# Kernel tuning notes

Hardware: AMD Instinct MI355X
Metric: run time of the kernel (lower is better)

## Reference

```python
import jax, jax.numpy as jnp
import numpy as np

J, F_ = 17, 32  # joints x per-joint features; C = J*F_ = 544
H = 8           # num_heads
EPS = 1e-5


def _layernorm(x, g, b):
    mu = jnp.mean(x, axis=-1, keepdims=True)
    var = jnp.mean((x - mu) ** 2, axis=-1, keepdims=True)
    return (x - mu) * jax.lax.rsqrt(var + EPS) * g + b


def setup_inputs() -> dict:
    key = jax.random.key(0)
    ks = jax.random.split(key, 8)
    B, N, C = 8, 1024, J * F_
    x = jax.random.normal(ks[0], (B, N, C), dtype=jnp.float32)
    s = 1.0 / np.sqrt(C)
    return {
        "x": x,
        "norm_g": jnp.ones((F_,), jnp.float32),
        "norm_b": jnp.zeros((F_,), jnp.float32),
        "ap_w": jax.random.normal(ks[1], (1, F_), jnp.float32) / np.sqrt(F_),
        "ap_b": jnp.zeros((1,), jnp.float32),
        "norm2_g": jnp.ones((C,), jnp.float32),
        "norm2_b": jnp.zeros((C,), jnp.float32),
        "qkv_w": jax.random.normal(ks[2], (3 * C, C), jnp.float32) * s,
        "proj_w": jax.random.normal(ks[3], (C, C), jnp.float32) * s,
        "proj_b": jnp.zeros((C,), jnp.float32),
        "scaling_factor": jnp.array([2.0], jnp.float32),
    }


def reference(x, norm_g, norm_b, ap_w, ap_b, norm2_g, norm2_b, qkv_w, proj_w, proj_b, scaling_factor):
    B, N, C = x.shape
    hd = C // H
    # --- attention pooling over joints ---
    xr = x.reshape(B, N, J, F_)
    xr = _layernorm(xr, norm_g, norm_b)                      # [B,N,17,32]
    scores = jnp.einsum('bnjf,of->bnjo', xr, ap_w)[..., 0] + ap_b[0]  # [B,N,17]
    # nn.Softmax(dim=1): softmax over sequence axis N (faithful to source)
    w = jax.nn.softmax(scores, axis=1)
    xp = (xr * w[..., None]).reshape(B, N, C)
    xp = _layernorm(xp, norm2_g, norm2_b)
    # --- position-scaled self-attention ---
    positions = jnp.linspace(0.0, 1.0, N, dtype=jnp.float32)  # [N]
    pos_scale = jnp.exp(-scaling_factor[0] * (positions - 0.5) ** 2)  # per-key scale
    qkv = (xp @ qkv_w.T).reshape(B, N, 3, H, hd)
    q = qkv[:, :, 0].transpose(0, 2, 1, 3)  # [B,H,N,hd]
    k = qkv[:, :, 1].transpose(0, 2, 1, 3)
    v = qkv[:, :, 2].transpose(0, 2, 1, 3)
    scale = hd ** -0.5
    attn = jnp.einsum('bhqd,bhkd->bhqk', q, k) * (scale * pos_scale[None, None, None, :])
    attn = jax.nn.softmax(attn, axis=-1)
    out = jnp.einsum('bhqk,bhkd->bhqd', attn, v)
    out = out.transpose(0, 2, 1, 3).reshape(B, N, C)
    return out @ proj_w.T + proj_b
```

## Files before the change

### kernel.cpp

```cpp
#include <hip/hip_runtime.h>
#include <hip/hip_bf16.h>

#define BB 8
#define NN 1024
#define CC 544
#define JJ 17
#define FF 32
#define HH 8
#define HD 68
#define BN 8192
#define KD 544
#define NCQ 1632
#define NCQP 1664
#define NCPP 640
#define NKB 9
#define BHSZ 73728
#define AQR 64

using f32x4  = __attribute__((ext_vector_type(4))) float;
using bf16x8 = __attribute__((ext_vector_type(8))) short;

__device__ __forceinline__ void gld_lds16(const void* g, void* l) {
  __builtin_amdgcn_global_load_lds(
      (const __attribute__((address_space(1))) void*)g,
      (__attribute__((address_space(3))) void*)l, 16, 0, 0);
}

__device__ __forceinline__ float bf16bits2f(short bits) {
  return __uint_as_float(((unsigned)(unsigned short)bits) << 16);
}

__global__ __launch_bounds__(256) void wconv_ln1(const float* __restrict__ x,
                                                 const float* __restrict__ g,
                                                 const float* __restrict__ bta,
                                                 const float* __restrict__ apw,
                                                 const float* __restrict__ apb,
                                                 __hip_bfloat16* __restrict__ xr,
                                                 float* __restrict__ scores,
                                                 const float* __restrict__ qkv_w,
                                                 const float* __restrict__ proj_w,
                                                 __hip_bfloat16* __restrict__ qw,
                                                 __hip_bfloat16* __restrict__ pw) {
  int bid = blockIdx.x, t = threadIdx.x;
  if (bid < BN / 4) {
    int wv = t >> 6, lane = t & 63;
    int bn = bid * 4 + wv;
    int f = lane & 31, half = lane >> 5;
    const float* row = x + (size_t)bn * CC;
    float gg = g[f], bb = bta[f], aw = apw[f], ab = apb[0];
    for (int it = 0; it < 9; ++it) {
      int j = it * 2 + half;
      bool act = (j < JJ);
      float v = act ? row[j * FF + f] : 0.f;
      float s = v;
      for (int m = 16; m >= 1; m >>= 1) s += __shfl_xor(s, m);
      float mu = s * (1.f / 32.f);
      float dv = v - mu;
      float s2 = dv * dv;
      for (int m = 16; m >= 1; m >>= 1) s2 += __shfl_xor(s2, m);
      float xn = dv * rsqrtf(s2 * (1.f / 32.f) + 1e-5f) * gg + bb;
      float sc = xn * aw;
      for (int m = 16; m >= 1; m >>= 1) sc += __shfl_xor(sc, m);
      if (act) {
        xr[(size_t)bn * CC + j * FF + f] = __float2bfloat16(xn);
        if (f == 0) scores[bn * JJ + j] = sc + ab;
      }
    }
  } else {
    int wb = bid - BN / 4;
    bool isq = wb < NCQP;
    int r = isq ? wb : wb - NCQP;
    const float* src = isq ? qkv_w : proj_w;
    __hip_bfloat16* dst = isq ? qw : pw;
    int nrows = isq ? NCQ : CC;
    if (t < KD / 4) {
      int c = t * 4;
      float4 v;
      if (r < nrows) v = *(const float4*)(src + (size_t)r * KD + c);
      else           v = float4{0.f, 0.f, 0.f, 0.f};
      __hip_bfloat16 o[4] = {__float2bfloat16(v.x), __float2bfloat16(v.y),
                             __float2bfloat16(v.z), __float2bfloat16(v.w)};
      *(unsigned long long*)(dst + (size_t)r * KD + c) = *(unsigned long long*)o;
    }
  }
}

__global__ __launch_bounds__(256) void softmax_red(const float* __restrict__ scores,
                                                   float2* __restrict__ tab) {
  int bj = blockIdx.x;
  int b = bj / JJ, j = bj - b * JJ;
  const float* s = scores + (size_t)b * NN * JJ + j;
  int t = threadIdx.x;
  float v[4];
  float mx = -1e30f;
#pragma unroll
  for (int i = 0; i < 4; ++i) { v[i] = s[(t + 256 * i) * JJ]; mx = fmaxf(mx, v[i]); }
#pragma unroll
  for (int m = 32; m >= 1; m >>= 1) mx = fmaxf(mx, __shfl_xor(mx, m));
  __shared__ float red[4];
  if ((t & 63) == 0) red[t >> 6] = mx;
  __syncthreads();
  mx = fmaxf(fmaxf(red[0], red[1]), fmaxf(red[2], red[3]));
  float sum = 0.f;
#pragma unroll
  for (int i = 0; i < 4; ++i) sum += __expf(v[i] - mx);
#pragma unroll
  for (int m = 32; m >= 1; m >>= 1) sum += __shfl_xor(sum, m);
  __shared__ float red2[4];
  if ((t & 63) == 0) red2[t >> 6] = sum;
  __syncthreads();
  if (t == 0) {
    sum = red2[0] + red2[1] + red2[2] + red2[3];
    tab[bj] = make_float2(mx, 1.f / sum);
  }
}

__global__ __launch_bounds__(256) void ln2_xp(const __hip_bfloat16* __restrict__ xr,
                                              const float* __restrict__ scores,
                                              const float2* __restrict__ tab,
                                              const float* __restrict__ g2,
                                              const float* __restrict__ b2,
                                              __hip_bfloat16* __restrict__ xp) {
  __shared__ float wsh[4][JJ];
  int wv = threadIdx.x >> 6, lane = threadIdx.x & 63;
  int bn = blockIdx.x * 4 + wv;
  if (lane < JJ) {
    float sc = scores[bn * JJ + lane];
    float2 mi = tab[(bn >> 10) * JJ + lane];
    wsh[wv][lane] = __expf(sc - mi.x) * mi.y;
  }
  const __hip_bfloat16* row = xr + (size_t)bn * CC;
  const bool has2 = (lane < 4);
  bf16x8 c0 = *(const bf16x8*)(row + lane * 8);
  bf16x8 c1 = {};
  if (has2) c1 = *(const bf16x8*)(row + (64 + lane) * 8);
  float w0 = wsh[wv][lane >> 2];
  float w1 = wsh[wv][16];
  float v0[8], v1[8];
  float sum = 0.f;
#pragma unroll
  for (int i = 0; i < 8; ++i) {
    v0[i] = bf16bits2f(c0[i]) * w0;
    sum += v0[i];
  }
#pragma unroll
  for (int i = 0; i < 8; ++i) {
    v1[i] = has2 ? bf16bits2f(c1[i]) * w1 : 0.f;
    sum += v1[i];
  }
  for (int m = 32; m >= 1; m >>= 1) sum += __shfl_xor(sum, m);
  float mu = sum * (1.f / 544.f);
  float s2 = 0.f;
#pragma unroll
  for (int i = 0; i < 8; ++i) { float dv = v0[i] - mu; s2 += dv * dv; }
  if (has2) {
#pragma unroll
    for (int i = 0; i < 8; ++i) { float dv = v1[i] - mu; s2 += dv * dv; }
  }
  for (int m = 32; m >= 1; m >>= 1) s2 += __shfl_xor(s2, m);
  float rstd = rsqrtf(s2 * (1.f / 544.f) + 1e-5f);
  __hip_bfloat16* dst = xp + (size_t)bn * CC;
  {
    float4 ga = *(const float4*)(g2 + lane * 8);
    float4 gb = *(const float4*)(g2 + lane * 8 + 4);
    float4 ba = *(const float4*)(b2 + lane * 8);
    float4 bb4 = *(const float4*)(b2 + lane * 8 + 4);
    float gg[8] = {ga.x, ga.y, ga.z, ga.w, gb.x, gb.y, gb.z, gb.w};
    float bbv[8] = {ba.x, ba.y, ba.z, ba.w, bb4.x, bb4.y, bb4.z, bb4.w};
    bf16x8 o;
#pragma unroll
    for (int i = 0; i < 8; ++i) {
      __hip_bfloat16 h = __float2bfloat16((v0[i] - mu) * rstd * gg[i] + bbv[i]);
      o[i] = *(short*)&h;
    }
    *(bf16x8*)(dst + lane * 8) = o;
  }
  if (has2) {
    float4 ga = *(const float4*)(g2 + 512 + lane * 8);
    float4 gb = *(const float4*)(g2 + 512 + lane * 8 + 4);
    float4 ba = *(const float4*)(b2 + 512 + lane * 8);
    float4 bb4 = *(const float4*)(b2 + 512 + lane * 8 + 4);
    float gg[8] = {ga.x, ga.y, ga.z, ga.w, gb.x, gb.y, gb.z, gb.w};
    float bbv[8] = {ba.x, ba.y, ba.z, ba.w, bb4.x, bb4.y, bb4.z, bb4.w};
    bf16x8 o;
#pragma unroll
    for (int i = 0; i < 8; ++i) {
      __hip_bfloat16 h = __float2bfloat16((v1[i] - mu) * rstd * gg[i] + bbv[i]);
      o[i] = *(short*)&h;
    }
    *(bf16x8*)(dst + 512 + lane * 8) = o;
  }
}

template <int MODE>
__global__ __launch_bounds__(256) void gemm_nt(const __hip_bfloat16* __restrict__ A,
                                               const __hip_bfloat16* __restrict__ Bw,
                                               __hip_bfloat16* __restrict__ Qp,
                                               __hip_bfloat16* __restrict__ Kp,
                                               __hip_bfloat16* __restrict__ Vt,
                                               float* __restrict__ Cf,
                                               const float* __restrict__ bias,
                                               const float* __restrict__ sfp) {
  extern __shared__ char smem[];
  __hip_bfloat16 (*As)[128 * 32] = (__hip_bfloat16 (*)[128 * 32])(smem);
  __hip_bfloat16 (*Bs)[128 * 32] = (__hip_bfloat16 (*)[128 * 32])(smem + 16384);
  const int t = threadIdx.x;
  const int w = t >> 6, lane = t & 63;
  const int fr = lane & 15, fq = lane >> 4;
  const int bi = blockIdx.x;
  constexpr int NBY = (MODE == 0) ? 13 : 5;
  const int xcd = bi & 7, q = bi >> 3;
  const int bxl = q / NBY, by = q - bxl * NBY;
  const int bx = xcd * 8 + bxl;
  const int m0 = bx * 128;
  const int n0 = by * 128;
  const int wm = (w >> 1) * 64, wn = (w & 1) * 64;

  f32x4 acc[4][4] = {};

  const __hip_bfloat16* Ag = A + (size_t)m0 * KD;
  const __hip_bfloat16* Bg = Bw + (size_t)n0 * KD;

#pragma unroll
  for (int i2 = 0; i2 < 2; ++i2) {
    int cb = (i2 * 4 + w) * 64;
    int chunk = cb + lane;
    int row = chunk >> 2, c16 = chunk & 3;
    gld_lds16(Ag + (size_t)row * KD + c16 * 8, &As[0][cb * 8]);
    gld_lds16(Bg + (size_t)row * KD + c16 * 8, &Bs[0][cb * 8]);
  }
  __syncthreads();

  for (int kt = 0; kt < 17; ++kt) {
    const int cur = kt & 1;
    if (kt < 16) {
      const int k0 = (kt + 1) * 32;
#pragma unroll
      for (int i2 = 0; i2 < 2; ++i2) {
        int cb = (i2 * 4 + w) * 64;
        int chunk = cb + lane;
        int row = chunk >> 2, c16 = chunk & 3;
        gld_lds16(Ag + (size_t)row * KD + k0 + c16 * 8, &As[1 - cur][cb * 8]);
        gld_lds16(Bg + (size_t)row * KD + k0 + c16 * 8, &Bs[1 - cur][cb * 8]);
      }
    }
    bf16x8 af[4], bfr[4];
#pragma unroll
    for (int tm = 0; tm < 4; ++tm)
      af[tm] = *(const bf16x8*)&As[cur][(wm + tm * 16 + fr) * 32 + fq * 8];
#pragma unroll
    for (int tn = 0; tn < 4; ++tn)
      bfr[tn] = *(const bf16x8*)&Bs[cur][(wn + tn * 16 + fr) * 32 + fq * 8];
#pragma unroll
    for (int tm = 0; tm < 4; ++tm)
#pragma unroll
      for (int tn = 0; tn < 4; ++tn)
        acc[tm][tn] = __builtin_amdgcn_mfma_f32_16x16x32_bf16(af[tm], bfr[tn], acc[tm][tn], 0, 0, 0);
    __syncthreads();
  }

  if (MODE == 1) {
#pragma unroll
    for (int tn = 0; tn < 4; ++tn) {
      int o = n0 + wn + tn * 16 + fr;
      if (o < CC) {
        float bb = bias[o];
#pragma unroll
        for (int tm = 0; tm < 4; ++tm) {
          int m = m0 + wm + tm * 16 + fq * 4;
#pragma unroll
          for (int r = 0; r < 4; ++r)
            Cf[(size_t)(m + r) * CC + o] = acc[tm][tn][r] + bb;
        }
      }
    }
  } else {
    const int b = m0 >> 10;
    const int nbase = m0 & (NN - 1);
    const float sf = sfp[0];
    __hip_bfloat16* Cst = (__hip_bfloat16*)smem;

#pragma unroll
    for (int tn = 0; tn < 4; ++tn) {
      int olocal = wn + tn * 16 + fr;
      int o = n0 + olocal;
      bool isk = (o >= CC) && (o < 2 * CC);
#pragma unroll
      for (int tm = 0; tm < 4; ++tm) {
        int mloc = wm + tm * 16 + fq * 4;
        int n = nbase + mloc;
#pragma unroll
        for (int r = 0; r < 4; ++r) {
          float v = acc[tm][tn][r];
          if (isk) {
            float pos = (n + r) * (1.f / 1023.f) - 0.5f;
            v *= __expf(-sf * pos * pos) * (0.12126781251816650f * 1.44269504088896340f);
          }
          Cst[olocal * 136 + mloc + r] = __float2bfloat16(v);
        }
      }
    }
    __syncthreads();

    for (int s = t; s < 32 * 128; s += 256) {
      int g = s >> 7, nl = s & 127;
      int o = n0 + g * 4;
      if (o < 2 * CC) {
        bool isk = o >= CC;
        int oo = isk ? o - CC : o;
        int h = oo / HD;
        int d0 = oo - h * HD;
        unsigned long long pk;
        __hip_bfloat16* pp = (__hip_bfloat16*)&pk;
#pragma unroll
        for (int j2 = 0; j2 < 4; ++j2) pp[j2] = Cst[(g * 4 + j2) * 136 + nl];
        __hip_bfloat16* basep = isk ? Kp : Qp;
        size_t ei = (size_t)(b * HH + h) * BHSZ + (size_t)(d0 >> 3) * (NN * 8) +
                    (size_t)(nbase + nl) * 8 + (d0 & 7);
        *(unsigned long long*)(basep + ei) = pk;
        if (d0 == 64) *(unsigned long long*)(basep + ei + 4) = 0ull;
      }
    }
    {
      int lo = 2 * CC - n0; if (lo < 0) lo = 0;
      int hi = NCQ - n0;    if (hi > 128) hi = 128;
      if (hi > lo) {
        int nv = hi - lo;
        for (int s = t; s < nv * 16; s += 256) {
          int row = lo + (s >> 4), seg = s & 15;
          int oo = n0 + row - 2 * CC;
          int h = oo / HD;
          int d = oo - h * HD;
          bf16x8 v8 = *(const bf16x8*)&Cst[row * 136 + seg * 8];
          __hip_bfloat16* vdst = Vt + ((size_t)(b * HH + h) * HD + d) * NN + nbase + seg * 8;
          *(bf16x8*)vdst = v8;
        }
      }
    }
  }
}

__global__ __launch_bounds__(128) void attn_kernel(const __hip_bfloat16* __restrict__ Qp,
                                                   const __hip_bfloat16* __restrict__ Kp,
                                                   const __hip_bfloat16* __restrict__ Vt,
                                                   __hip_bfloat16* __restrict__ Ao) {
  __shared__ __hip_bfloat16 Qs[NKB * 64 * 8];
  __shared__ __hip_bfloat16 Ks[2][NKB * 64 * 8];
  __shared__ __hip_bfloat16 Zs[64 * 8];
  const int t = threadIdx.x;
  const int w = t >> 6, lane = t & 63;
  const int fr = lane & 15, fq = lane >> 4;
  const int idx = blockIdx.x;
  const int bh = idx & 63, qt = idx >> 6;
  const int h = bh & 7, b = bh >> 3;

  const __hip_bfloat16* qtile = Qp + (size_t)bh * BHSZ + (size_t)qt * AQR * 8;
  const __hip_bfloat16* kbase = Kp + (size_t)bh * BHSZ;
  const __hip_bfloat16* vbase = Vt + (size_t)bh * HD * NN;

  *(unsigned long long*)&Zs[t * 4] = 0ull;
#pragma unroll
  for (int i = 0; i < 5; ++i) {
    int kb = i * 2 + w;
    if (kb < NKB) gld_lds16(qtile + (size_t)kb * (NN * 8) + lane * 8, &Qs[kb * 64 * 8]);
  }
#pragma unroll
  for (int i = 0; i < 5; ++i) {
    int kb = i * 2 + w;
    if (kb < NKB) gld_lds16(kbase + (size_t)kb * (NN * 8) + lane * 8, &Ks[0][kb * 64 * 8]);
  }
  __syncthreads();
  bf16x8 qa[2][3];
#pragma unroll
  for (int ks = 0; ks < 3; ++ks) {
    const __hip_bfloat16* qb = (ks < 2 || fq == 0) ? &Qs[(ks * 4 + fq) * 512] : Zs;
#pragma unroll
    for (int g = 0; g < 2; ++g)
      qa[g][ks] = *(const bf16x8*)&qb[(w * 32 + g * 16 + fr) * 8];
  }
  __syncthreads();

  f32x4 o_acc[2][5] = {};
  float l_part[2][4] = {};
  const int dclamp = (fr < 4) ? 0 : 1;

  for (int kt = 0; kt < 16; ++kt) {
    const int cur = kt & 1;
    bf16x8 vfrag[5][2];
#pragma unroll
    for (int tv = 0; tv < 5; ++tv) {
      int d = tv * 16 + fr;
      int dc = (tv == 4 && dclamp) ? 0 : d;
#pragma unroll
      for (int ks2 = 0; ks2 < 2; ++ks2)
        vfrag[tv][ks2] = *(const bf16x8*)(vbase + (size_t)dc * NN + kt * 64 + ks2 * 32 + fq * 8);
    }
    if (kt < 15) {
      const __hip_bfloat16* ktile = kbase + (size_t)(kt + 1) * 64 * 8;
#pragma unroll
      for (int i = 0; i < 5; ++i) {
        int kb = i * 2 + w;
        if (kb < NKB) gld_lds16(ktile + (size_t)kb * (NN * 8) + lane * 8, &Ks[1 - cur][kb * 64 * 8]);
      }
    }

    f32x4 s[2][4] = {};
#pragma unroll
    for (int ks = 0; ks < 3; ++ks) {
      const __hip_bfloat16* kbL = (ks < 2 || fq == 0) ? &Ks[cur][(ks * 4 + fq) * 512] : Zs;
#pragma unroll
      for (int tn = 0; tn < 4; ++tn) {
        bf16x8 kb = *(const bf16x8*)&kbL[(tn * 16 + fr) * 8];
        s[0][tn] = __builtin_amdgcn_mfma_f32_16x16x32_bf16(qa[0][ks], kb, s[0][tn], 0, 0, 0);
        s[1][tn] = __builtin_amdgcn_mfma_f32_16x16x32_bf16(qa[1][ks], kb, s[1][tn], 0, 0, 0);
      }
    }
#pragma unroll
    for (int g = 0; g < 2; ++g) {
      __hip_bfloat16* Pw = &Qs[(w * 2 + g) * 1152];
#pragma unroll
      for (int tn = 0; tn < 4; ++tn)
#pragma unroll
        for (int r = 0; r < 4; ++r) {
          float pe = __builtin_amdgcn_exp2f(s[g][tn][r]);
          l_part[g][r] += pe;
          Pw[(fq * 4 + r) * 72 + tn * 16 + fr] = __float2bfloat16(pe);
        }
    }
#pragma unroll
    for (int ks2 = 0; ks2 < 2; ++ks2) {
      bf16x8 pa0 = *(const bf16x8*)&Qs[(w * 2 + 0) * 1152 + fr * 72 + ks2 * 32 + fq * 8];
      bf16x8 pa1 = *(const bf16x8*)&Qs[(w * 2 + 1) * 1152 + fr * 72 + ks2 * 32 + fq * 8];
#pragma unroll
      for (int tv = 0; tv < 5; ++tv) {
        o_acc[0][tv] = __builtin_amdgcn_mfma_f32_16x16x32_bf16(pa0, vfrag[tv][ks2], o_acc[0][tv], 0, 0, 0);
        o_acc[1][tv] = __builtin_amdgcn_mfma_f32_16x16x32_bf16(pa1, vfrag[tv][ks2], o_acc[1][tv], 0, 0, 0);
      }
    }
    __syncthreads();
  }
#pragma unroll
  for (int g = 0; g < 2; ++g) {
    __hip_bfloat16* obase = Ao + (size_t)(b * NN + qt * AQR + w * 32 + g * 16) * CC + h * HD;
    float inv[4];
#pragma unroll
    for (int r = 0; r < 4; ++r) {
      float l = l_part[g][r];
#pragma unroll
      for (int msk = 8; msk >= 1; msk >>= 1) l += __shfl_xor(l, msk);
      inv[r] = 1.f / l;
    }
#pragma unroll
    for (int tv = 0; tv < 5; ++tv) {
      int d = tv * 16 + fr;
      if (d < HD) {
#pragma unroll
        for (int r = 0; r < 4; ++r)
          obase[(size_t)(fq * 4 + r) * CC + d] = __float2bfloat16(o_acc[g][tv][r] * inv[r]);
      }
    }
  }
}

extern "C" void kernel_launch(void* const* d_in, const int* in_sizes, int n_in,
                              void* d_out, int out_size, void* d_ws, size_t ws_size,
                              hipStream_t stream) {
  (void)in_sizes; (void)n_in; (void)out_size; (void)ws_size;
  const float* x       = (const float*)d_in[0];
  const float* norm_g  = (const float*)d_in[1];
  const float* norm_b  = (const float*)d_in[2];
  const float* ap_w    = (const float*)d_in[3];
  const float* ap_b    = (const float*)d_in[4];
  const float* norm2_g = (const float*)d_in[5];
  const float* norm2_b = (const float*)d_in[6];
  const float* qkv_w   = (const float*)d_in[7];
  const float* proj_w  = (const float*)d_in[8];
  const float* proj_b  = (const float*)d_in[9];
  const float* sf      = (const float*)d_in[10];
  float* out = (float*)d_out;
  char* ws = (char*)d_ws;

  __hip_bfloat16* xr   = (__hip_bfloat16*)(ws);
  float* scores        = (float*)(ws + 8912896);
  float2* tab          = (float2*)(ws + 9469952);
  __hip_bfloat16* xp   = (__hip_bfloat16*)(ws + 9474048);
  __hip_bfloat16* qw   = (__hip_bfloat16*)(ws + 18386944);
  __hip_bfloat16* pw   = (__hip_bfloat16*)(ws + 20197376);
  __hip_bfloat16* vt   = (__hip_bfloat16*)(ws + 20893696);
  __hip_bfloat16* ao   = (__hip_bfloat16*)(ws + 29806592);
  __hip_bfloat16* qp   = (__hip_bfloat16*)(ws + 38719488);
  __hip_bfloat16* kp   = (__hip_bfloat16*)(ws + 48156672);

  wconv_ln1<<<BN / 4 + NCQP + NCPP, 256, 0, stream>>>(
      x, norm_g, norm_b, ap_w, ap_b, xr, scores, qkv_w, proj_w, qw, pw);
  softmax_red<<<BB * JJ, 256, 0, stream>>>(scores, tab);
  ln2_xp<<<BN / 4, 256, 0, stream>>>(xr, scores, tab, norm2_g, norm2_b, xp);
  gemm_nt<0><<<dim3(64 * 13), 256, 34816, stream>>>(xp, qw, qp, kp, vt, nullptr, nullptr, sf);
  attn_kernel<<<dim3((NN / AQR) * HH * BB), 128, 0, stream>>>(qp, kp, vt, ao);
  gemm_nt<1><<<dim3(64 * 5), 256, 34816, stream>>>(ao, pw, nullptr, nullptr, nullptr, out, proj_b, nullptr);
}
```

Before: 199.6 us.

## Use per-wave private K buffers to drop block barriers in attention loop

Each wave now loads its own double-buffered copy of the first eight K blocks into LDS and reads the ninth K block straight from global memory. Q fragments are loaded directly into registers instead of being staged through LDS. Together these remove every __syncthreads from the key loop, using a manual vmcnt wait plus a sched barrier instead. The cost is double the K global/LDS traffic, since both waves fetch the same K, and reliance on a hand-counted vmcnt that is fragile. Without a barrier, correctness of the per-wave P buffer reuse and the LDS async-load visibility depends on that wait count being right.

```diff
diff --git a/kernel.cpp b/kernel.cpp
--- a/kernel.cpp
+++ b/kernel.cpp
@@ -344,9 +344,8 @@
                                                    const __hip_bfloat16* __restrict__ Kp,
                                                    const __hip_bfloat16* __restrict__ Vt,
                                                    __hip_bfloat16* __restrict__ Ao) {
-  __shared__ __hip_bfloat16 Qs[NKB * 64 * 8];
-  __shared__ __hip_bfloat16 Ks[2][NKB * 64 * 8];
-  __shared__ __hip_bfloat16 Zs[64 * 8];
+  __shared__ __hip_bfloat16 Kpriv[2][2][8 * 64 * 8];
+  __shared__ __hip_bfloat16 Pw[2][1152];
   const int t = threadIdx.x;
   const int w = t >> 6, lane = t & 63;
   const int fr = lane & 15, fq = lane >> 4;
@@ -354,31 +353,29 @@
   const int bh = idx & 63, qt = idx >> 6;
   const int h = bh & 7, b = bh >> 3;
 
-  const __hip_bfloat16* qtile = Qp + (size_t)bh * BHSZ + (size_t)qt * AQR * 8;
+  const __hip_bfloat16* qbase = Qp + (size_t)bh * BHSZ;
   const __hip_bfloat16* kbase = Kp + (size_t)bh * BHSZ;
   const __hip_bfloat16* vbase = Vt + (size_t)bh * HD * NN;
-
-  *(unsigned long long*)&Zs[t * 4] = 0ull;
-#pragma unroll
-  for (int i = 0; i < 5; ++i) {
-    int kb = i * 2 + w;
-    if (kb < NKB) gld_lds16(qtile + (size_t)kb * (NN * 8) + lane * 8, &Qs[kb * 64 * 8]);
-  }
-#pragma unroll
-  for (int i = 0; i < 5; ++i) {
-    int kb = i * 2 + w;
-    if (kb < NKB) gld_lds16(kbase + (size_t)kb * (NN * 8) + lane * 8, &Ks[0][kb * 64 * 8]);
-  }
-  __syncthreads();
+  const __hip_bfloat16* k8base = kbase + (size_t)8 * (NN * 8);
+
+  const bf16x8 zero8 = {};
+
   bf16x8 qa[2][3];
 #pragma unroll
   for (int ks = 0; ks < 3; ++ks) {
-    const __hip_bfloat16* qb = (ks < 2 || fq == 0) ? &Qs[(ks * 4 + fq) * 512] : Zs;
-#pragma unroll
-    for (int g = 0; g < 2; ++g)
-      qa[g][ks] = *(const bf16x8*)&qb[(w * 32 + g * 16 + fr) * 8];
-  }
-  __syncthreads();
+    int kblk = ks * 4 + fq;
+#pragma unroll
+    for (int g = 0; g < 2; ++g) {
+      bf16x8 v = zero8;
+      if (kblk <= 8)
+        v = *(const bf16x8*)(qbase + (size_t)kblk * (NN * 8) +
+                             ((size_t)qt * AQR + w * 32 + g * 16 + fr) * 8);
+      qa[g][ks] = v;
+    }
+  }
+#pragma unroll
+  for (int kb = 0; kb < 8; ++kb)
+    gld_lds16(kbase + (size_t)kb * (NN * 8) + lane * 8, &Kpriv[w][0][kb * 512]);
 
   f32x4 o_acc[2][5] = {};
   float l_part[2][4] = {};
@@ -395,49 +392,55 @@
       for (int ks2 = 0; ks2 < 2; ++ks2)
         vfrag[tv][ks2] = *(const bf16x8*)(vbase + (size_t)dc * NN + kt * 64 + ks2 * 32 + fq * 8);
     }
-    if (kt < 15) {
-      const __hip_bfloat16* ktile = kbase + (size_t)(kt + 1) * 64 * 8;
-#pragma unroll
-      for (int i = 0; i < 5; ++i) {
-        int kb = i * 2 + w;
-        if (kb < NKB) gld_lds16(ktile + (size_t)kb * (NN * 8) + lane * 8, &Ks[1 - cur][kb * 64 * 8]);
-      }
-    }
-
-    f32x4 s[2][4] = {};
-#pragma unroll
-    for (int ks = 0; ks < 3; ++ks) {
-      const __hip_bfloat16* kbL = (ks < 2 || fq == 0) ? &Ks[cur][(ks * 4 + fq) * 512] : Zs;
-#pragma unroll
-      for (int tn = 0; tn < 4; ++tn) {
-        bf16x8 kb = *(const bf16x8*)&kbL[(tn * 16 + fr) * 8];
-        s[0][tn] = __builtin_amdgcn_mfma_f32_16x16x32_bf16(qa[0][ks], kb, s[0][tn], 0, 0, 0);
-        s[1][tn] = __builtin_amdgcn_mfma_f32_16x16x32_bf16(qa[1][ks], kb, s[1][tn], 0, 0, 0);
-      }
-    }
+    bf16x8 k8[4];
+#pragma unroll
+    for (int tn = 0; tn < 4; ++tn) {
+      bf16x8 v = zero8;
+      if (fq == 0)
+        v = *(const bf16x8*)(k8base + ((size_t)kt * 64 + tn * 16 + fr) * 8);
+      k8[tn] = v;
+    }
+    {
+      const int ktn = (kt + 1) & 15;
+      const __hip_bfloat16* ktile = kbase + (size_t)ktn * 64 * 8;
+#pragma unroll
+      for (int kb = 0; kb < 8; ++kb)
+        gld_lds16(ktile + (size_t)kb * (NN * 8) + lane * 8, &Kpriv[w][1 - cur][kb * 512]);
+    }
+    asm volatile("s_waitcnt vmcnt(22)" ::: "memory");
+    __builtin_amdgcn_sched_barrier(0);
+
 #pragma unroll
     for (int g = 0; g < 2; ++g) {
-      __hip_bfloat16* Pw = &Qs[(w * 2 + g) * 1152];
+      f32x4 s[4] = {};
+#pragma unroll
+      for (int ks = 0; ks < 2; ++ks) {
+        const __hip_bfloat16* kbL = &Kpriv[w][cur][(ks * 4 + fq) * 512];
+#pragma unroll
+        for (int tn = 0; tn < 4; ++tn) {
+          bf16x8 kb = *(const bf16x8*)&kbL[(tn * 16 + fr) * 8];
+          s[tn] = __builtin_amdgcn_mfma_f32_16x16x32_bf16(qa[g][ks], kb, s[tn], 0, 0, 0);
+        }
+      }
 #pragma unroll
       for (int tn = 0; tn < 4; ++tn)
+        s[tn] = __builtin_amdgcn_mfma_f32_16x16x32_bf16(qa[g][2], k8[tn], s[tn], 0, 0, 0);
+#pragma unroll
+      for (int tn = 0; tn < 4; ++tn)
 #pragma unroll
         for (int r = 0; r < 4; ++r) {
-          float pe = __builtin_amdgcn_exp2f(s[g][tn][r]);
+          float pe = __builtin_amdgcn_exp2f(s[tn][r]);
           l_part[g][r] += pe;
-          Pw[(fq * 4 + r) * 72 + tn * 16 + fr] = __float2bfloat16(pe);
+          Pw[w][(fq * 4 + r) * 72 + tn * 16 + fr] = __float2bfloat16(pe);
         }
-    }
-#pragma unroll
-    for (int ks2 = 0; ks2 < 2; ++ks2) {
-      bf16x8 pa0 = *(const bf16x8*)&Qs[(w * 2 + 0) * 1152 + fr * 72 + ks2 * 32 + fq * 8];
-      bf16x8 pa1 = *(const bf16x8*)&Qs[(w * 2 + 1) * 1152 + fr * 72 + ks2 * 32 + fq * 8];
-#pragma unroll
-      for (int tv = 0; tv < 5; ++tv) {
-        o_acc[0][tv] = __builtin_amdgcn_mfma_f32_16x16x32_bf16(pa0, vfrag[tv][ks2], o_acc[0][tv], 0, 0, 0);
-        o_acc[1][tv] = __builtin_amdgcn_mfma_f32_16x16x32_bf16(pa1, vfrag[tv][ks2], o_acc[1][tv], 0, 0, 0);
-      }
-    }
-    __syncthreads();
+#pragma unroll
+      for (int ks2 = 0; ks2 < 2; ++ks2) {
+        bf16x8 pa = *(const bf16x8*)&Pw[w][fr * 72 + ks2 * 32 + fq * 8];
+#pragma unroll
+        for (int tv = 0; tv < 5; ++tv)
+          o_acc[g][tv] = __builtin_amdgcn_mfma_f32_16x16x32_bf16(pa, vfrag[tv][ks2], o_acc[g][tv], 0, 0, 0);
+      }
+    }
   }
 #pragma unroll
   for (int g = 0; g < 2; ++g) {
```

After: 206.7 us. +3.6%, slower.
